# Kernel tuning notes

Hardware: AMD Instinct MI355X
Metric: run time of the kernel (lower is better)

The kernel has to match this reference:

```python
import jax, jax.numpy as jnp
import numpy as np

B = 2048       # number of samples
A = 64         # max agents per sample (static)
E = 128        # h_dim
H = 8          # num_heads
DH = E // H    # head dim = 16


def _agents():
    # deterministic ragged pattern covering 1..64; sum = 66560
    return jnp.asarray(((np.arange(B) * 7) % A) + 1, dtype=jnp.int32)


def setup_inputs() -> dict:
    key = jax.random.key(0)
    ks = jax.random.split(key, 6)
    agents = _agents()
    total = int(np.sum(((np.arange(B) * 7) % A) + 1))  # 66560
    att_in = jax.random.normal(ks[0], (total, E), dtype=jnp.float32)
    # nn.MultiheadAttention parameters
    in_proj_w = jax.random.normal(ks[1], (3 * E, E), dtype=jnp.float32) * 0.02
    in_proj_b = jnp.zeros((3 * E,), dtype=jnp.float32)
    out_proj_w = jax.random.normal(ks[2], (E, E), dtype=jnp.float32) * 0.02
    out_proj_b = jnp.zeros((E,), dtype=jnp.float32)
    return {
        "att_in": att_in,
        "in_proj_w": in_proj_w,
        "in_proj_b": in_proj_b,
        "out_proj_w": out_proj_w,
        "out_proj_b": out_proj_b,
        "agents_per_sample": agents,
    }


def reference(att_in, in_proj_w, in_proj_b, out_proj_w, out_proj_b, agents_per_sample):
    total = att_in.shape[0]
    # ---- pad ragged [total, E] -> [B, A, E] ----
    sample_ids = jnp.repeat(jnp.arange(B), agents_per_sample, total_repeat_length=total)
    offsets = jnp.concatenate([jnp.zeros((1,), jnp.int32), jnp.cumsum(agents_per_sample)[:-1]])
    slot_ids = jnp.arange(total) - offsets[sample_ids]
    padded = jnp.zeros((B, A, E), att_in.dtype).at[sample_ids, slot_ids].set(att_in)
    key_valid = jnp.arange(A)[None, :] < agents_per_sample[:, None]  # [B, A]

    # ---- multi-head self-attention (dropout disabled / eval mode) ----
    qkv = padded @ in_proj_w.T + in_proj_b            # [B, A, 3E]
    q, k, v = jnp.split(qkv, 3, axis=-1)
    def heads(x):
        return x.reshape(B, A, H, DH).transpose(0, 2, 1, 3)  # [B, H, A, DH]
    q, k, v = heads(q), heads(k), heads(v)
    scores = jnp.einsum("bhqd,bhkd->bhqk", q, k) / jnp.sqrt(jnp.float32(DH))
    scores = jnp.where(key_valid[:, None, None, :], scores, jnp.float32(-1e9))
    attn = jax.nn.softmax(scores, axis=-1)            # [B, H, A, A]
    ctx = jnp.einsum("bhqk,bhkd->bhqd", attn, v)      # [B, H, A, DH]
    ctx = ctx.transpose(0, 2, 1, 3).reshape(B, A, E)
    out = ctx @ out_proj_w.T + out_proj_b             # [B, A, E]

    # ---- unpad back to flat ragged [total, E] ----
    return out[sample_ids, slot_ids]
```

## Files before the change

### kernel.cpp

```cpp
#include <hip/hip_runtime.h>

#define NB    2048
#define AMAX  64
#define EDIM  128
#define TOTAL 66560
#define DHEAD 16
#define KVSTR 20
#define XSTR  129
#define LSTR  136
#define WELEM 65536

typedef _Float16 f16x8 __attribute__((ext_vector_type(8)));
typedef _Float16 f16x4 __attribute__((ext_vector_type(4)));
typedef float    f32x4 __attribute__((ext_vector_type(4)));

__global__ __launch_bounds__(256) void prep_kernel(const int* __restrict__ ag,
                                                   int* __restrict__ offs,
                                                   const float* __restrict__ win,
                                                   const float* __restrict__ wout,
                                                   _Float16* __restrict__ wh) {
    if (blockIdx.x == 0) {
        __shared__ int part[256];
        const int t = threadIdx.x;
        int loc[8];
        int s = 0;
#pragma unroll
        for (int i = 0; i < 8; ++i) { loc[i] = s; s += ag[t * 8 + i]; }
        part[t] = s;
        __syncthreads();
        for (int d = 1; d < 256; d <<= 1) {
            int v = (t >= d) ? part[t - d] : 0;
            __syncthreads();
            part[t] += v;
            __syncthreads();
        }
        const int base = (t == 0) ? 0 : part[t - 1];
#pragma unroll
        for (int i = 0; i < 8; ++i) offs[t * 8 + i] = base + loc[i];
    } else {
        const int base = (blockIdx.x - 1) * 1024 + threadIdx.x * 4;
        const float4 v = (base < 49152) ? *(const float4*)(win + base)
                                        : *(const float4*)(wout + (base - 49152));
        f16x4 h;
        h[0] = (_Float16)v.x; h[1] = (_Float16)v.y;
        h[2] = (_Float16)v.z; h[3] = (_Float16)v.w;
        *(f16x4*)(wh + base) = h;
    }
}

__global__ __launch_bounds__(256, 2) void fused_attn_kernel(
    const float*    __restrict__ x,
    const _Float16* __restrict__ winh,
    const float*    __restrict__ bin,
    const _Float16* __restrict__ woh,
    const float*    __restrict__ bout,
    const int*      __restrict__ ag,
    const int*      __restrict__ offs,
    float*          __restrict__ out)
{
    __shared__ __align__(16) _Float16 xs[AMAX * LSTR];

    const int i    = blockIdx.x;
    const int b    = (((63 - (i >> 5)) * 55) & 63) + ((i & 31) << 6);
    const int n    = ag[b];
    const int off  = offs[b];
    const int tid  = threadIdx.x;
    const int lane = tid & 63;
    const int wid  = __builtin_amdgcn_readfirstlane(tid >> 6);
    const int l15  = lane & 15;
    const int quad = lane >> 4;
    const int nt   = (n + 15) >> 4;

#pragma unroll
    for (int it = 0; it < 4; ++it) {
        const int u = it * 256 + tid;
        const int r = u >> 4, c8 = u & 15;
        f16x8 hv = {};
        if (r < n) {
            const float4 a0 = *(const float4*)(x + (size_t)(off + r) * EDIM + c8 * 8);
            const float4 a1 = *(const float4*)(x + (size_t)(off + r) * EDIM + c8 * 8 + 4);
            hv[0]=(_Float16)a0.x; hv[1]=(_Float16)a0.y; hv[2]=(_Float16)a0.z; hv[3]=(_Float16)a0.w;
            hv[4]=(_Float16)a1.x; hv[5]=(_Float16)a1.y; hv[6]=(_Float16)a1.z; hv[7]=(_Float16)a1.w;
        }
        *(f16x8*)(xs + r * LSTR + c8 * 8) = hv;
    }
    __syncthreads();

    f16x8 wq[2][4], wk[2][4], wv[2][4];
    float bqa[2][4], bka[2][4], bva[2];
#pragma unroll
    for (int m = 0; m < 2; ++m) {
        const int h = wid * 2 + m;
#pragma unroll
        for (int ks = 0; ks < 4; ++ks) {
            wq[m][ks] = *(const f16x8*)(winh + (size_t)(h * 16 + l15) * EDIM + ks * 32 + quad * 8);
            wk[m][ks] = *(const f16x8*)(winh + (size_t)(128 + h * 16 + l15) * EDIM + ks * 32 + quad * 8);
            wv[m][ks] = *(const f16x8*)(winh + (size_t)(256 + h * 16 + l15) * EDIM + ks * 32 + quad * 8);
        }
        const float4 bq = *(const float4*)(bin + h * 16 + quad * 4);
        const float4 bk = *(const float4*)(bin + 128 + h * 16 + quad * 4);
        bqa[m][0]=bq.x; bqa[m][1]=bq.y; bqa[m][2]=bq.z; bqa[m][3]=bq.w;
        bka[m][0]=bk.x; bka[m][1]=bk.y; bka[m][2]=bk.z; bka[m][3]=bk.w;
        bva[m] = bin[256 + h * 16 + l15];
    }

    f16x4 qf[2][4], kf[2][4], vf[2][4];
#pragma unroll
    for (int kt = 0; kt < 4; ++kt) if (kt < nt) {
        f16x8 xf[4];
#pragma unroll
        for (int ks = 0; ks < 4; ++ks)
            xf[ks] = *(const f16x8*)(xs + (kt * 16 + l15) * LSTR + ks * 32 + quad * 8);
#pragma unroll
        for (int m = 0; m < 2; ++m) {
            f32x4 aq = (f32x4){0.f,0.f,0.f,0.f};
            f32x4 ak = (f32x4){0.f,0.f,0.f,0.f};
            f32x4 av = (f32x4){0.f,0.f,0.f,0.f};
#pragma unroll
            for (int ks = 0; ks < 4; ++ks) {
                aq = __builtin_amdgcn_mfma_f32_16x16x32_f16(wq[m][ks], xf[ks], aq, 0, 0, 0);
                ak = __builtin_amdgcn_mfma_f32_16x16x32_f16(wk[m][ks], xf[ks], ak, 0, 0, 0);
                av = __builtin_amdgcn_mfma_f32_16x16x32_f16(xf[ks], wv[m][ks], av, 0, 0, 0);
            }
#pragma unroll
            for (int r = 0; r < 4; ++r) {
                qf[m][kt][r] = (_Float16)((aq[r] + bqa[m][r]) * 0.25f);
                kf[m][kt][r] = (_Float16)(ak[r] + bka[m][r]);
                vf[m][kt][r] = (_Float16)(av[r] + bva[m]);
            }
        }
    }

    f16x4 ctxf[2][4] = {};
#pragma unroll
    for (int qt = 0; qt < 4; ++qt) if (qt < nt) {
        f32x4 sv0[4], sv1[4];
#pragma unroll
        for (int kt = 0; kt < 4; ++kt) if (kt < nt) {
            sv0[kt] = __builtin_amdgcn_mfma_f32_16x16x16f16(
                          kf[0][kt], qf[0][qt], (f32x4){0.f,0.f,0.f,0.f}, 0, 0, 0);
            sv1[kt] = __builtin_amdgcn_mfma_f32_16x16x16f16(
                          kf[1][kt], qf[1][qt], (f32x4){0.f,0.f,0.f,0.f}, 0, 0, 0);
        }
        float ls0 = 0.f, ls1 = 0.f;
#pragma unroll
        for (int kt = 0; kt < 4; ++kt) if (kt < nt) {
#pragma unroll
            for (int r = 0; r < 4; ++r) {
                const int key = kt * 16 + quad * 4 + r;
                const float p0 = (key < n) ? __expf(sv0[kt][r]) : 0.f;
                const float p1 = (key < n) ? __expf(sv1[kt][r]) : 0.f;
                ls0 += p0; sv0[kt][r] = p0;
                ls1 += p1; sv1[kt][r] = p1;
            }
        }
        ls0 += __shfl_xor(ls0, 16, 64);
        ls1 += __shfl_xor(ls1, 16, 64);
        ls0 += __shfl_xor(ls0, 32, 64);
        ls1 += __shfl_xor(ls1, 32, 64);
        const float inv0 = 1.0f / ls0;
        const float inv1 = 1.0f / ls1;
        f16x4 pf0[4], pf1[4];
#pragma unroll
        for (int kt = 0; kt < 4; ++kt) if (kt < nt) {
#pragma unroll
            for (int r = 0; r < 4; ++r) {
                pf0[kt][r] = (_Float16)(sv0[kt][r] * inv0);
                pf1[kt][r] = (_Float16)(sv1[kt][r] * inv1);
            }
        }
        f32x4 a0A = (f32x4){0.f,0.f,0.f,0.f}, a0B = (f32x4){0.f,0.f,0.f,0.f};
        f32x4 a1A = (f32x4){0.f,0.f,0.f,0.f}, a1B = (f32x4){0.f,0.f,0.f,0.f};
#pragma unroll
        for (int kt = 0; kt < 4; ++kt) if (kt < nt) {
            if ((kt & 1) == 0) {
                a0A = __builtin_amdgcn_mfma_f32_16x16x16f16(pf0[kt], vf[0][kt], a0A, 0, 0, 0);
                a1A = __builtin_amdgcn_mfma_f32_16x16x16f16(pf1[kt], vf[1][kt], a1A, 0, 0, 0);
            } else {
                a0B = __builtin_amdgcn_mfma_f32_16x16x16f16(pf0[kt], vf[0][kt], a0B, 0, 0, 0);
                a1B = __builtin_amdgcn_mfma_f32_16x16x16f16(pf1[kt], vf[1][kt], a1B, 0, 0, 0);
            }
        }
#pragma unroll
        for (int r = 0; r < 4; ++r) {
            ctxf[0][qt][r] = (_Float16)(a0A[r] + a0B[r]);
            ctxf[1][qt][r] = (_Float16)(a1A[r] + a1B[r]);
        }
    }

    __syncthreads();
#pragma unroll
    for (int m = 0; m < 2; ++m) {
        const int h = wid * 2 + m;
#pragma unroll
        for (int qt = 0; qt < 4; ++qt) if (qt < nt) {
#pragma unroll
            for (int r = 0; r < 4; ++r)
                xs[(qt * 16 + quad * 4 + r) * LSTR + h * 16 + l15] = ctxf[m][qt][r];
        }
    }
    __syncthreads();

    {
        f32x4 oacc[4][2];
#pragma unroll
        for (int t = 0; t < 4; ++t) { oacc[t][0] = (f32x4){0.f,0.f,0.f,0.f}; oacc[t][1] = (f32x4){0.f,0.f,0.f,0.f}; }
#pragma unroll
        for (int ks = 0; ks < 4; ++ks) {
            f16x8 cf[2];
#pragma unroll
            for (int c2 = 0; c2 < 2; ++c2)
                cf[c2] = *(const f16x8*)(woh + (wid * 32 + c2 * 16 + l15) * EDIM + ks * 32 + quad * 8);
#pragma unroll
            for (int t = 0; t < 4; ++t) if (t < nt) {
                const f16x8 rf = *(const f16x8*)(xs + (t * 16 + l15) * LSTR + ks * 32 + quad * 8);
                oacc[t][0] = __builtin_amdgcn_mfma_f32_16x16x32_f16(cf[0], rf, oacc[t][0], 0, 0, 0);
                oacc[t][1] = __builtin_amdgcn_mfma_f32_16x16x32_f16(cf[1], rf, oacc[t][1], 0, 0, 0);
            }
        }
        const float4 bo0 = *(const float4*)(bout + wid * 32 + quad * 4);
        const float4 bo1 = *(const float4*)(bout + wid * 32 + 16 + quad * 4);
#pragma unroll
        for (int t = 0; t < 4; ++t) if (t < nt) {
            const int row = t * 16 + l15;
            if (row < n) {
                float* orow = out + (size_t)(off + row) * EDIM + wid * 32;
                *(float4*)(orow + quad * 4) =
                    make_float4(oacc[t][0][0] + bo0.x, oacc[t][0][1] + bo0.y,
                                oacc[t][0][2] + bo0.z, oacc[t][0][3] + bo0.w);
                *(float4*)(orow + 16 + quad * 4) =
                    make_float4(oacc[t][1][0] + bo1.x, oacc[t][1][1] + bo1.y,
                                oacc[t][1][2] + bo1.z, oacc[t][1][3] + bo1.w);
            }
        }
    }
}

__global__ __launch_bounds__(256, 2) void attn_fused_kernel(
    const float* __restrict__ x, const float* __restrict__ win,
    const float* __restrict__ bin, const float* __restrict__ wout,
    const float* __restrict__ bout, const int* __restrict__ ag,
    const int* __restrict__ offs, float* __restrict__ out)
{
    __shared__ __align__(16) float xs[AMAX * XSTR];
    __shared__ __align__(16) float kvs[8][AMAX * KVSTR];
    const int b = blockIdx.x, n = ag[b], off = offs[b];
    const int tid = threadIdx.x, lane = tid & 63;
    const int wid = __builtin_amdgcn_readfirstlane(tid >> 6);
#pragma unroll
    for (int it = 0; it < 8; ++it) {
        const int f4 = it * 256 + tid;
        const int r = f4 >> 5, c = (f4 & 31) << 2;
        float4 v = make_float4(0.f, 0.f, 0.f, 0.f);
        if (r < n) v = *(const float4*)(x + (size_t)(off + r) * EDIM + c);
        float* d = xs + r * XSTR + c;
        d[0]=v.x; d[1]=v.y; d[2]=v.z; d[3]=v.w;
    }
    __syncthreads();
    float* kw = kvs[wid*2+0]; float* vw = kvs[wid*2+1];
    const float* xrow = xs + lane * XSTR;
    float ctxk[2][DHEAD];
#pragma unroll
    for (int m = 0; m < 2; ++m) {
        const int h = wid * 2 + m;
        float qa[DHEAD], ka[DHEAD], va[DHEAD];
#pragma unroll
        for (int d = 0; d < DHEAD; ++d) { qa[d]=0.f; ka[d]=0.f; va[d]=0.f; }
        const float* wq = win + (size_t)(h*DHEAD)*EDIM;
        const float* wk = win + (size_t)(EDIM + h*DHEAD)*EDIM;
        const float* wv = win + (size_t)(2*EDIM + h*DHEAD)*EDIM;
        for (int k = 0; k < EDIM; ++k) {
            const float xv = xrow[k];
#pragma unroll
            for (int d = 0; d < DHEAD; ++d) {
                qa[d] = fmaf(xv, wq[d*EDIM+k], qa[d]);
                ka[d] = fmaf(xv, wk[d*EDIM+k], ka[d]);
                va[d] = fmaf(xv, wv[d*EDIM+k], va[d]);
            }
        }
#pragma unroll
        for (int d = 0; d < DHEAD; ++d) {
            qa[d] = (qa[d] + bin[h*DHEAD+d]) * 0.25f;
            ka[d] += bin[EDIM + h*DHEAD + d];
            va[d] += bin[2*EDIM + h*DHEAD + d];
        }
#pragma unroll
        for (int d = 0; d < DHEAD; ++d) { kw[lane*KVSTR+d] = ka[d]; vw[lane*KVSTR+d] = va[d]; }
        float mrun = -1e30f, lrun = 0.f, cacc[DHEAD];
#pragma unroll
        for (int d = 0; d < DHEAD; ++d) cacc[d] = 0.f;
        const int nch = (n + 15) >> 4;
        for (int ch = 0; ch < nch; ++ch) {
            const int jb = ch << 4;
            float s[16], p[16];
#pragma unroll
            for (int jj = 0; jj < 16; ++jj) {
                const float4* kr = (const float4*)(kw + (jb + jj) * KVSTR);
                const float4 k0=kr[0],k1=kr[1],k2=kr[2],k3=kr[3];
                const float kk[16] = {k0.x,k0.y,k0.z,k0.w,k1.x,k1.y,k1.z,k1.w,
                                      k2.x,k2.y,k2.z,k2.w,k3.x,k3.y,k3.z,k3.w};
                float a = 0.f;
#pragma unroll
                for (int d = 0; d < DHEAD; ++d) a = fmaf(qa[d], kk[d], a);
                s[jj] = (jb + jj < n) ? a : -1e30f;
            }
            float mc = s[0];
#pragma unroll
            for (int jj = 1; jj < 16; ++jj) mc = fmaxf(mc, s[jj]);
            const float mnew = fmaxf(mrun, mc);
            const float alpha = __expf(mrun - mnew);
            float psum = 0.f;
#pragma unroll
            for (int jj = 0; jj < 16; ++jj) { p[jj] = __expf(s[jj]-mnew); psum += p[jj]; }
            lrun = fmaf(lrun, alpha, psum);
#pragma unroll
            for (int d = 0; d < DHEAD; ++d) cacc[d] *= alpha;
#pragma unroll
            for (int jj = 0; jj < 16; ++jj) {
                const float4* vr = (const float4*)(vw + (jb + jj) * KVSTR);
                const float4 v0=vr[0],v1=vr[1],v2=vr[2],v3=vr[3];
                const float vv[16] = {v0.x,v0.y,v0.z,v0.w,v1.x,v1.y,v1.z,v1.w,
                                      v2.x,v2.y,v2.z,v2.w,v3.x,v3.y,v3.z,v3.w};
                const float pj = p[jj];
#pragma unroll
                for (int d = 0; d < DHEAD; ++d) cacc[d] = fmaf(pj, vv[d], cacc[d]);
            }
            mrun = mnew;
        }
        const float inv = 1.0f / lrun;
#pragma unroll
        for (int d = 0; d < DHEAD; ++d) ctxk[m][d] = cacc[d] * inv;
    }
    __syncthreads();
#pragma unroll
    for (int m = 0; m < 2; ++m) {
        const int h = wid * 2 + m;
#pragma unroll
        for (int d = 0; d < DHEAD; ++d) xs[lane*XSTR + h*DHEAD + d] = ctxk[m][d];
    }
    __syncthreads();
    const int c0 = wid * 32;
#pragma unroll
    for (int ct = 0; ct < 4; ++ct) {
        const int cc = c0 + ct * 8;
        float a8[8];
#pragma unroll
        for (int j = 0; j < 8; ++j) a8[j] = 0.f;
#pragma unroll 4
        for (int e = 0; e < EDIM; ++e) {
            const float cv = xrow[e];
#pragma unroll
            for (int j = 0; j < 8; ++j) a8[j] = fmaf(cv, wout[(size_t)(cc+j)*EDIM+e], a8[j]);
        }
        if (lane < n) {
            float* orow = out + (size_t)(off + lane) * EDIM + cc;
#pragma unroll
            for (int j = 0; j < 8; ++j) orow[j] = a8[j] + bout[cc+j];
        }
    }
}

extern "C" void kernel_launch(void* const* d_in, const int* in_sizes, int n_in,
                              void* d_out, int out_size, void* d_ws, size_t ws_size,
                              hipStream_t stream) {
    const float* x   = (const float*)d_in[0];
    const float* win = (const float*)d_in[1];
    const float* bin = (const float*)d_in[2];
    const float* wo  = (const float*)d_in[3];
    const float* bo  = (const float*)d_in[4];
    const int*   ag  = (const int*)d_in[5];
    float* out = (float*)d_out;

    const size_t need = (size_t)WELEM * sizeof(_Float16) + NB * sizeof(int);
    if (ws_size >= need) {
        _Float16* wh = (_Float16*)d_ws;
        int* offs = (int*)(wh + WELEM);
        prep_kernel<<<65, 256, 0, stream>>>(ag, offs, win, wo, wh);
        fused_attn_kernel<<<NB, 256, 0, stream>>>(x, wh, bin, wh + 49152, bo, ag, offs, out);
    } else {
        int* offs = (int*)d_ws;
        prep_kernel<<<1, 256, 0, stream>>>(ag, offs, nullptr, nullptr, nullptr);
        attn_fused_kernel<<<NB, 256, 0, stream>>>(x, win, bin, wo, bo, ag, offs, out);
    }
}
```

Baseline: 141.3 us.

## Fold prep kernel into fused attention: in-block offset scan and on-the-fly weight conversion

Removes the separate prep launch. Each block now computes its own ragged offset with a block-wide reduction over agent counts, and converts fp32 weights to fp16 inline at load time. The QKV projection loop is reordered to iterate over the K-slices on the outside, so weight fragments are loaded per slice instead of all being held in registers up front. In exchange, every block redundantly reads 2048 agent counts and re-converts the weights, and more accumulators stay live. The softmax sum is also split into per-tile partial sums, and the fallback scalar kernel is deleted.

```diff
diff --git a/kernel.cpp b/kernel.cpp
--- a/kernel.cpp
+++ b/kernel.cpp
@@ -5,71 +5,58 @@
 #define EDIM  128
 #define TOTAL 66560
 #define DHEAD 16
-#define KVSTR 20
-#define XSTR  129
 #define LSTR  136
-#define WELEM 65536
 
 typedef _Float16 f16x8 __attribute__((ext_vector_type(8)));
 typedef _Float16 f16x4 __attribute__((ext_vector_type(4)));
 typedef float    f32x4 __attribute__((ext_vector_type(4)));
 
-__global__ __launch_bounds__(256) void prep_kernel(const int* __restrict__ ag,
-                                                   int* __restrict__ offs,
-                                                   const float* __restrict__ win,
-                                                   const float* __restrict__ wout,
-                                                   _Float16* __restrict__ wh) {
-    if (blockIdx.x == 0) {
-        __shared__ int part[256];
-        const int t = threadIdx.x;
-        int loc[8];
-        int s = 0;
-#pragma unroll
-        for (int i = 0; i < 8; ++i) { loc[i] = s; s += ag[t * 8 + i]; }
-        part[t] = s;
-        __syncthreads();
-        for (int d = 1; d < 256; d <<= 1) {
-            int v = (t >= d) ? part[t - d] : 0;
-            __syncthreads();
-            part[t] += v;
-            __syncthreads();
-        }
-        const int base = (t == 0) ? 0 : part[t - 1];
-#pragma unroll
-        for (int i = 0; i < 8; ++i) offs[t * 8 + i] = base + loc[i];
-    } else {
-        const int base = (blockIdx.x - 1) * 1024 + threadIdx.x * 4;
-        const float4 v = (base < 49152) ? *(const float4*)(win + base)
-                                        : *(const float4*)(wout + (base - 49152));
-        f16x4 h;
-        h[0] = (_Float16)v.x; h[1] = (_Float16)v.y;
-        h[2] = (_Float16)v.z; h[3] = (_Float16)v.w;
-        *(f16x4*)(wh + base) = h;
-    }
+static __device__ __forceinline__ f16x8 ldcvt8(const float* __restrict__ p) {
+    const float4 a0 = *(const float4*)p;
+    const float4 a1 = *(const float4*)(p + 4);
+    f16x8 h;
+    h[0]=(_Float16)a0.x; h[1]=(_Float16)a0.y; h[2]=(_Float16)a0.z; h[3]=(_Float16)a0.w;
+    h[4]=(_Float16)a1.x; h[5]=(_Float16)a1.y; h[6]=(_Float16)a1.z; h[7]=(_Float16)a1.w;
+    return h;
 }
 
 __global__ __launch_bounds__(256, 2) void fused_attn_kernel(
-    const float*    __restrict__ x,
-    const _Float16* __restrict__ winh,
-    const float*    __restrict__ bin,
-    const _Float16* __restrict__ woh,
-    const float*    __restrict__ bout,
-    const int*      __restrict__ ag,
-    const int*      __restrict__ offs,
-    float*          __restrict__ out)
+    const float* __restrict__ x,
+    const float* __restrict__ win,
+    const float* __restrict__ bin,
+    const float* __restrict__ wout,
+    const float* __restrict__ bout,
+    const int*   __restrict__ ag,
+    float*       __restrict__ out)
 {
     __shared__ __align__(16) _Float16 xs[AMAX * LSTR];
+    __shared__ int offp[4];
 
     const int i    = blockIdx.x;
     const int b    = (((63 - (i >> 5)) * 55) & 63) + ((i & 31) << 6);
-    const int n    = ag[b];
-    const int off  = offs[b];
     const int tid  = threadIdx.x;
     const int lane = tid & 63;
     const int wid  = __builtin_amdgcn_readfirstlane(tid >> 6);
     const int l15  = lane & 15;
     const int quad = lane >> 4;
-    const int nt   = (n + 15) >> 4;
+
+    int pacc = 0;
+    {
+        const int base8 = tid * 8;
+#pragma unroll
+        for (int j = 0; j < 8; ++j) {
+            const int idx = base8 + j;
+            const int v = ag[idx];
+            pacc += (idx < b) ? v : 0;
+        }
+#pragma unroll
+        for (int d = 1; d < 64; d <<= 1) pacc += __shfl_xor(pacc, d, 64);
+        if (lane == 0) offp[wid] = pacc;
+    }
+    const int n  = ag[b];
+    const int nt = (n + 15) >> 4;
+    __syncthreads();
+    const int off = offp[0] + offp[1] + offp[2] + offp[3];
 
 #pragma unroll
     for (int it = 0; it < 4; ++it) {
@@ -86,17 +73,10 @@
     }
     __syncthreads();
 
-    f16x8 wq[2][4], wk[2][4], wv[2][4];
     float bqa[2][4], bka[2][4], bva[2];
 #pragma unroll
     for (int m = 0; m < 2; ++m) {
         const int h = wid * 2 + m;
-#pragma unroll
-        for (int ks = 0; ks < 4; ++ks) {
-            wq[m][ks] = *(const f16x8*)(winh + (size_t)(h * 16 + l15) * EDIM + ks * 32 + quad * 8);
-            wk[m][ks] = *(const f16x8*)(winh + (size_t)(128 + h * 16 + l15) * EDIM + ks * 32 + quad * 8);
-            wv[m][ks] = *(const f16x8*)(winh + (size_t)(256 + h * 16 + l15) * EDIM + ks * 32 + quad * 8);
-        }
         const float4 bq = *(const float4*)(bin + h * 16 + quad * 4);
         const float4 bk = *(const float4*)(bin + 128 + h * 16 + quad * 4);
         bqa[m][0]=bq.x; bqa[m][1]=bq.y; bqa[m][2]=bq.z; bqa[m][3]=bq.w;
@@ -104,32 +84,47 @@
         bva[m] = bin[256 + h * 16 + l15];
     }
 
+    f32x4 aq[2][4], ak[2][4], av[2][4];
+#pragma unroll
+    for (int m = 0; m < 2; ++m)
+#pragma unroll
+        for (int kt = 0; kt < 4; ++kt) {
+            aq[m][kt] = (f32x4){0.f,0.f,0.f,0.f};
+            ak[m][kt] = (f32x4){0.f,0.f,0.f,0.f};
+            av[m][kt] = (f32x4){0.f,0.f,0.f,0.f};
+        }
+#pragma unroll
+    for (int ks = 0; ks < 4; ++ks) {
+        f16x8 xf[4];
+#pragma unroll
+        for (int kt = 0; kt < 4; ++kt) if (kt < nt)
+            xf[kt] = *(const f16x8*)(xs + (kt * 16 + l15) * LSTR + ks * 32 + quad * 8);
+#pragma unroll
+        for (int m = 0; m < 2; ++m) {
+            const int h = wid * 2 + m;
+            const f16x8 wqf = ldcvt8(win + (size_t)(h * 16 + l15) * EDIM + ks * 32 + quad * 8);
+            const f16x8 wkf = ldcvt8(win + (size_t)(128 + h * 16 + l15) * EDIM + ks * 32 + quad * 8);
+            const f16x8 wvf = ldcvt8(win + (size_t)(256 + h * 16 + l15) * EDIM + ks * 32 + quad * 8);
+#pragma unroll
+            for (int kt = 0; kt < 4; ++kt) if (kt < nt) {
+                aq[m][kt] = __builtin_amdgcn_mfma_f32_16x16x32_f16(wqf, xf[kt], aq[m][kt], 0, 0, 0);
+                ak[m][kt] = __builtin_amdgcn_mfma_f32_16x16x32_f16(wkf, xf[kt], ak[m][kt], 0, 0, 0);
+                av[m][kt] = __builtin_amdgcn_mfma_f32_16x16x32_f16(xf[kt], wvf, av[m][kt], 0, 0, 0);
+            }
+        }
+    }
     f16x4 qf[2][4], kf[2][4], vf[2][4];
 #pragma unroll
-    for (int kt = 0; kt < 4; ++kt) if (kt < nt) {
-        f16x8 xf[4];
-#pragma unroll
-        for (int ks = 0; ks < 4; ++ks)
-            xf[ks] = *(const f16x8*)(xs + (kt * 16 + l15) * LSTR + ks * 32 + quad * 8);
-#pragma unroll
-        for (int m = 0; m < 2; ++m) {
-            f32x4 aq = (f32x4){0.f,0.f,0.f,0.f};
-            f32x4 ak = (f32x4){0.f,0.f,0.f,0.f};
-            f32x4 av = (f32x4){0.f,0.f,0.f,0.f};
-#pragma unroll
-            for (int ks = 0; ks < 4; ++ks) {
-                aq = __builtin_amdgcn_mfma_f32_16x16x32_f16(wq[m][ks], xf[ks], aq, 0, 0, 0);
-                ak = __builtin_amdgcn_mfma_f32_16x16x32_f16(wk[m][ks], xf[ks], ak, 0, 0, 0);
-                av = __builtin_amdgcn_mfma_f32_16x16x32_f16(xf[ks], wv[m][ks], av, 0, 0, 0);
-            }
+    for (int m = 0; m < 2; ++m)
+#pragma unroll
+        for (int kt = 0; kt < 4; ++kt) if (kt < nt) {
 #pragma unroll
             for (int r = 0; r < 4; ++r) {
-                qf[m][kt][r] = (_Float16)((aq[r] + bqa[m][r]) * 0.25f);
-                kf[m][kt][r] = (_Float16)(ak[r] + bka[m][r]);
-                vf[m][kt][r] = (_Float16)(av[r] + bva[m]);
-            }
-        }
-    }
+                qf[m][kt][r] = (_Float16)((aq[m][kt][r] + bqa[m][r]) * 0.25f);
+                kf[m][kt][r] = (_Float16)(ak[m][kt][r] + bka[m][r]);
+                vf[m][kt][r] = (_Float16)(av[m][kt][r] + bva[m]);
+            }
+        }
 
     f16x4 ctxf[2][4] = {};
 #pragma unroll
@@ -142,18 +137,24 @@
             sv1[kt] = __builtin_amdgcn_mfma_f32_16x16x16f16(
                           kf[1][kt], qf[1][qt], (f32x4){0.f,0.f,0.f,0.f}, 0, 0, 0);
         }
-        float ls0 = 0.f, ls1 = 0.f;
-#pragma unroll
-        for (int kt = 0; kt < 4; ++kt) if (kt < nt) {
+        float t0[4], t1[4];
+#pragma unroll
+        for (int kt = 0; kt < 4; ++kt) { t0[kt] = 0.f; t1[kt] = 0.f; }
+#pragma unroll
+        for (int kt = 0; kt < 4; ++kt) if (kt < nt) {
+            float s0 = 0.f, s1 = 0.f;
 #pragma unroll
             for (int r = 0; r < 4; ++r) {
                 const int key = kt * 16 + quad * 4 + r;
                 const float p0 = (key < n) ? __expf(sv0[kt][r]) : 0.f;
                 const float p1 = (key < n) ? __expf(sv1[kt][r]) : 0.f;
-                ls0 += p0; sv0[kt][r] = p0;
-                ls1 += p1; sv1[kt][r] = p1;
-            }
-        }
+                s0 += p0; sv0[kt][r] = p0;
+                s1 += p1; sv1[kt][r] = p1;
+            }
+            t0[kt] = s0; t1[kt] = s1;
+        }
+        float ls0 = (t0[0] + t0[1]) + (t0[2] + t0[3]);
+        float ls1 = (t1[0] + t1[1]) + (t1[2] + t1[3]);
         ls0 += __shfl_xor(ls0, 16, 64);
         ls1 += __shfl_xor(ls1, 16, 64);
         ls0 += __shfl_xor(ls0, 32, 64);
@@ -207,15 +208,13 @@
         for (int t = 0; t < 4; ++t) { oacc[t][0] = (f32x4){0.f,0.f,0.f,0.f}; oacc[t][1] = (f32x4){0.f,0.f,0.f,0.f}; }
 #pragma unroll
         for (int ks = 0; ks < 4; ++ks) {
-            f16x8 cf[2];
-#pragma unroll
-            for (int c2 = 0; c2 < 2; ++c2)
-                cf[c2] = *(const f16x8*)(woh + (wid * 32 + c2 * 16 + l15) * EDIM + ks * 32 + quad * 8);
+            const f16x8 cf0 = ldcvt8(wout + (size_t)(wid * 32 + l15) * EDIM + ks * 32 + quad * 8);
+            const f16x8 cf1 = ldcvt8(wout + (size_t)(wid * 32 + 16 + l15) * EDIM + ks * 32 + quad * 8);
 #pragma unroll
             for (int t = 0; t < 4; ++t) if (t < nt) {
                 const f16x8 rf = *(const f16x8*)(xs + (t * 16 + l15) * LSTR + ks * 32 + quad * 8);
-                oacc[t][0] = __builtin_amdgcn_mfma_f32_16x16x32_f16(cf[0], rf, oacc[t][0], 0, 0, 0);
-                oacc[t][1] = __builtin_amdgcn_mfma_f32_16x16x32_f16(cf[1], rf, oacc[t][1], 0, 0, 0);
+                oacc[t][0] = __builtin_amdgcn_mfma_f32_16x16x32_f16(cf0, rf, oacc[t][0], 0, 0, 0);
+                oacc[t][1] = __builtin_amdgcn_mfma_f32_16x16x32_f16(cf1, rf, oacc[t][1], 0, 0, 0);
             }
         }
         const float4 bo0 = *(const float4*)(bout + wid * 32 + quad * 4);
@@ -236,130 +235,6 @@
     }
 }
 
-__global__ __launch_bounds__(256, 2) void attn_fused_kernel(
-    const float* __restrict__ x, const float* __restrict__ win,
-    const float* __restrict__ bin, const float* __restrict__ wout,
-    const float* __restrict__ bout, const int* __restrict__ ag,
-    const int* __restrict__ offs, float* __restrict__ out)
-{
-    __shared__ __align__(16) float xs[AMAX * XSTR];
-    __shared__ __align__(16) float kvs[8][AMAX * KVSTR];
-    const int b = blockIdx.x, n = ag[b], off = offs[b];
-    const int tid = threadIdx.x, lane = tid & 63;
-    const int wid = __builtin_amdgcn_readfirstlane(tid >> 6);
-#pragma unroll
-    for (int it = 0; it < 8; ++it) {
-        const int f4 = it * 256 + tid;
-        const int r = f4 >> 5, c = (f4 & 31) << 2;
-        float4 v = make_float4(0.f, 0.f, 0.f, 0.f);
-        if (r < n) v = *(const float4*)(x + (size_t)(off + r) * EDIM + c);
-        float* d = xs + r * XSTR + c;
-        d[0]=v.x; d[1]=v.y; d[2]=v.z; d[3]=v.w;
-    }
-    __syncthreads();
-    float* kw = kvs[wid*2+0]; float* vw = kvs[wid*2+1];
-    const float* xrow = xs + lane * XSTR;
-    float ctxk[2][DHEAD];
-#pragma unroll
-    for (int m = 0; m < 2; ++m) {
-        const int h = wid * 2 + m;
-        float qa[DHEAD], ka[DHEAD], va[DHEAD];
-#pragma unroll
-        for (int d = 0; d < DHEAD; ++d) { qa[d]=0.f; ka[d]=0.f; va[d]=0.f; }
-        const float* wq = win + (size_t)(h*DHEAD)*EDIM;
-        const float* wk = win + (size_t)(EDIM + h*DHEAD)*EDIM;
-        const float* wv = win + (size_t)(2*EDIM + h*DHEAD)*EDIM;
-        for (int k = 0; k < EDIM; ++k) {
-            const float xv = xrow[k];
-#pragma unroll
-            for (int d = 0; d < DHEAD; ++d) {
-                qa[d] = fmaf(xv, wq[d*EDIM+k], qa[d]);
-                ka[d] = fmaf(xv, wk[d*EDIM+k], ka[d]);
-                va[d] = fmaf(xv, wv[d*EDIM+k], va[d]);
-            }
-        }
-#pragma unroll
-        for (int d = 0; d < DHEAD; ++d) {
-            qa[d] = (qa[d] + bin[h*DHEAD+d]) * 0.25f;
-            ka[d] += bin[EDIM + h*DHEAD + d];
-            va[d] += bin[2*EDIM + h*DHEAD + d];
-        }
-#pragma unroll
-        for (int d = 0; d < DHEAD; ++d) { kw[lane*KVSTR+d] = ka[d]; vw[lane*KVSTR+d] = va[d]; }
-        float mrun = -1e30f, lrun = 0.f, cacc[DHEAD];
-#pragma unroll
-        for (int d = 0; d < DHEAD; ++d) cacc[d] = 0.f;
-        const int nch = (n + 15) >> 4;
-        for (int ch = 0; ch < nch; ++ch) {
-            const int jb = ch << 4;
-            float s[16], p[16];
-#pragma unroll
-            for (int jj = 0; jj < 16; ++jj) {
-                const float4* kr = (const float4*)(kw + (jb + jj) * KVSTR);
-                const float4 k0=kr[0],k1=kr[1],k2=kr[2],k3=kr[3];
-                const float kk[16] = {k0.x,k0.y,k0.z,k0.w,k1.x,k1.y,k1.z,k1.w,
-                                      k2.x,k2.y,k2.z,k2.w,k3.x,k3.y,k3.z,k3.w};
-                float a = 0.f;
-#pragma unroll
-                for (int d = 0; d < DHEAD; ++d) a = fmaf(qa[d], kk[d], a);
-                s[jj] = (jb + jj < n) ? a : -1e30f;
-            }
-            float mc = s[0];
-#pragma unroll
-            for (int jj = 1; jj < 16; ++jj) mc = fmaxf(mc, s[jj]);
-            const float mnew = fmaxf(mrun, mc);
-            const float alpha = __expf(mrun - mnew);
-            float psum = 0.f;
-#pragma unroll
-            for (int jj = 0; jj < 16; ++jj) { p[jj] = __expf(s[jj]-mnew); psum += p[jj]; }
-            lrun = fmaf(lrun, alpha, psum);
-#pragma unroll
-            for (int d = 0; d < DHEAD; ++d) cacc[d] *= alpha;
-#pragma unroll
-            for (int jj = 0; jj < 16; ++jj) {
-                const float4* vr = (const float4*)(vw + (jb + jj) * KVSTR);
-                const float4 v0=vr[0],v1=vr[1],v2=vr[2],v3=vr[3];
-                const float vv[16] = {v0.x,v0.y,v0.z,v0.w,v1.x,v1.y,v1.z,v1.w,
-                                      v2.x,v2.y,v2.z,v2.w,v3.x,v3.y,v3.z,v3.w};
-                const float pj = p[jj];
-#pragma unroll
-                for (int d = 0; d < DHEAD; ++d) cacc[d] = fmaf(pj, vv[d], cacc[d]);
-            }
-            mrun = mnew;
-        }
-        const float inv = 1.0f / lrun;
-#pragma unroll
-        for (int d = 0; d < DHEAD; ++d) ctxk[m][d] = cacc[d] * inv;
-    }
-    __syncthreads();
-#pragma unroll
-    for (int m = 0; m < 2; ++m) {
-        const int h = wid * 2 + m;
-#pragma unroll
-        for (int d = 0; d < DHEAD; ++d) xs[lane*XSTR + h*DHEAD + d] = ctxk[m][d];
-    }
-    __syncthreads();
-    const int c0 = wid * 32;
-#pragma unroll
-    for (int ct = 0; ct < 4; ++ct) {
-        const int cc = c0 + ct * 8;
-        float a8[8];
-#pragma unroll
-        for (int j = 0; j < 8; ++j) a8[j] = 0.f;
-#pragma unroll 4
-        for (int e = 0; e < EDIM; ++e) {
-            const float cv = xrow[e];
-#pragma unroll
-            for (int j = 0; j < 8; ++j) a8[j] = fmaf(cv, wout[(size_t)(cc+j)*EDIM+e], a8[j]);
-        }
-        if (lane < n) {
-            float* orow = out + (size_t)(off + lane) * EDIM + cc;
-#pragma unroll
-            for (int j = 0; j < 8; ++j) orow[j] = a8[j] + bout[cc+j];
-        }
-    }
-}
-
 extern "C" void kernel_launch(void* const* d_in, const int* in_sizes, int n_in,
                               void* d_out, int out_size, void* d_ws, size_t ws_size,
                               hipStream_t stream) {
@@ -370,16 +245,7 @@
     const float* bo  = (const float*)d_in[4];
     const int*   ag  = (const int*)d_in[5];
     float* out = (float*)d_out;
-
-    const size_t need = (size_t)WELEM * sizeof(_Float16) + NB * sizeof(int);
-    if (ws_size >= need) {
-        _Float16* wh = (_Float16*)d_ws;
-        int* offs = (int*)(wh + WELEM);
-        prep_kernel<<<65, 256, 0, stream>>>(ag, offs, win, wo, wh);
-        fused_attn_kernel<<<NB, 256, 0, stream>>>(x, wh, bin, wh + 49152, bo, ag, offs, out);
-    } else {
-        int* offs = (int*)d_ws;
-        prep_kernel<<<1, 256, 0, stream>>>(ag, offs, nullptr, nullptr, nullptr);
-        attn_fused_kernel<<<NB, 256, 0, stream>>>(x, win, bin, wo, bo, ag, offs, out);
-    }
+    (void)d_ws; (void)ws_size;
+
+    fused_attn_kernel<<<NB, 256, 0, stream>>>(x, win, bin, wo, bo, ag, out);
 }
```

New measurement: 162.4 us. 14.9% more time.
